# Kernel optimization log

Measured on AMD Instinct MI355X. Metric: run time of the kernel, lower is better.

The kernel has to match this reference:

```python
import jax, jax.numpy as jnp
import numpy as np

N = 65536      # flattened tokens
K = 8192       # codebook_size
D = 64         # codebook_dim
DECAY = 0.9
EPS = 1e-05


def setup_inputs() -> dict:
    key = jax.random.key(0)
    k1, k2, k3, k4 = jax.random.split(key, 4)
    z = jax.random.normal(k1, (N, D), dtype=jnp.float32)
    # codebook initialized uniform(-1, 1) in the torch module
    weight = jax.random.uniform(k2, (K, D), dtype=jnp.float32, minval=-1.0, maxval=1.0)
    # EMA state: positive cluster sizes, embed_avg near the codebook
    cluster_size = jax.random.uniform(k3, (K,), dtype=jnp.float32)
    embed_avg = weight + 0.01 * jax.random.normal(k4, (K, D), dtype=jnp.float32)
    return {"z": z, "weight": weight, "cluster_size": cluster_size, "embed_avg": embed_avg}


def reference(z, weight, cluster_size, embed_avg):
    # VectorQuantizer.ema_update: distances -> argmin -> gather -> EMA stats -> weight refresh
    zd = jax.lax.stop_gradient(z)  # torch uses z.detach() for distance/quant_error
    # distance[n,k] = ||z_n||^2 + ||c_k||^2 - 2 z_n . c_k   (addmm pattern)
    dist = (zd * zd).sum(1, keepdims=True) + (weight * weight).sum(1) - 2.0 * (zd @ weight.T)  # [N, K]
    token = jnp.argmin(dist, axis=1)                      # [N]
    embed = weight[token]                                  # gather [N, D]
    quant_error = jnp.mean(((embed - zd) ** 2).sum(1))

    # onehot_probs.sum(0) == per-code counts; onehot.T @ z == segment sum of z
    counts = jax.ops.segment_sum(jnp.ones((zd.shape[0],), zd.dtype), token, num_segments=K)  # [K]
    embed_sum = jax.ops.segment_sum(z, token, num_segments=K)                                # [K, D]

    new_cluster_size = cluster_size * DECAY + (1.0 - DECAY) * counts
    new_embed_avg = embed_avg * DECAY + (1.0 - DECAY) * embed_sum

    # ema_weight_update with num_tokens = codebook_size
    n = new_cluster_size.sum()
    smoothed = (new_cluster_size + EPS) / (n + K * EPS) * n
    new_weight = new_embed_avg / smoothed[:, None]

    return quant_error, new_weight, new_cluster_size, new_embed_avg
```

## Files before the change

kernel.cpp:

```cpp
#include <hip/hip_runtime.h>
#include <type_traits>

#define N_TOK 65536
#define K_CODE 8192
#define D_DIM 64

constexpr float DECAY = 0.9f;
constexpr float OMD = 0.1f;
constexpr float EPS = 1e-5f;

constexpr int OUT_QE = 0;
constexpr int OUT_W  = 1;
constexpr int OUT_CS = 1 + K_CODE * D_DIM;
constexpr int OUT_EA = OUT_CS + K_CODE;

constexpr int WS_QE     = 0;
constexpr int WS_NSUM   = 16;
constexpr int WS_COUNTS = 16 + 8 * 32;
constexpr int WS_EMBSUM = WS_COUNTS + K_CODE;
constexpr int WS_WHI    = WS_EMBSUM + K_CODE * D_DIM;
constexpr int WS_WLO    = WS_WHI + K_CODE * D_DIM / 2;
constexpr int WS_CNF    = WS_WLO + K_CODE * D_DIM / 2;

typedef __attribute__((ext_vector_type(16))) float floatx16;
typedef __attribute__((ext_vector_type(8)))  short short8;
typedef __attribute__((ext_vector_type(8)))  __bf16 bf16x8;

template <typename T, typename = void> struct mfma_takes : std::false_type {};
template <typename T>
struct mfma_takes<T, std::void_t<decltype(__builtin_amdgcn_mfma_f32_32x32x16_bf16(
    std::declval<T>(), std::declval<T>(), std::declval<floatx16>(), 0, 0, 0))>>
    : std::true_type {};

__device__ __forceinline__ floatx16 MFMA(short8 a, short8 b, floatx16 c) {
  if constexpr (mfma_takes<bf16x8>::value) {
    return __builtin_amdgcn_mfma_f32_32x32x16_bf16(
        __builtin_bit_cast(bf16x8, a), __builtin_bit_cast(bf16x8, b), c, 0, 0, 0);
  } else {
    return __builtin_amdgcn_mfma_f32_32x32x16_bf16(a, b, c, 0, 0, 0);
  }
}

__device__ __forceinline__ unsigned short bf16rne(float x) {
  unsigned int u = __float_as_uint(x);
  return (unsigned short)((u + 0x7FFFu + ((u >> 16) & 1u)) >> 16);
}

__device__ __forceinline__ void gload_lds16(const unsigned short* g, unsigned short* l) {
#if defined(__has_builtin) && __has_builtin(__builtin_amdgcn_global_load_lds)
  typedef __attribute__((address_space(1))) void gvoid;
  typedef __attribute__((address_space(3))) void lvoid;
  __builtin_amdgcn_global_load_lds((gvoid*)g, (lvoid*)l, 16, 0, 0);
#else
  *(uint4*)l = *(const uint4*)g;
#endif
}

__global__ void vq_prep(const float* __restrict__ w, const float* __restrict__ cs,
                        float* __restrict__ ws) {
  const int tid = threadIdx.x;
  const int gid = blockIdx.x * 256 + tid;
  ws[WS_EMBSUM + gid] = 0.0f;
  if (gid < K_CODE) ws[WS_COUNTS + gid] = 0.0f;

  const int d = tid & 63;
  const int kw = tid >> 6;
  const int k = blockIdx.x * 4 + kw;
  const float v = w[(size_t)k * D_DIM + d];
  const unsigned short h = bf16rne(v);
  const float hf = __uint_as_float((unsigned int)h << 16);
  const unsigned short l = bf16rne(v - hf);
  unsigned short* whi = (unsigned short*)(ws + WS_WHI);
  unsigned short* wlo = (unsigned short*)(ws + WS_WLO);
  const int pos = k * D_DIM + (((d >> 3) ^ (k & 7)) * 8) + (d & 7);
  whi[pos] = h;
  wlo[pos] = l;
  float s = v * v;
#pragma unroll
  for (int m = 32; m >= 1; m >>= 1) s += __shfl_xor(s, m);
  __shared__ float csp[4];
  if (d == 0) {
    (ws + WS_CNF)[k] = s + 64.0f;
    csp[kw] = cs[k];
  }
  __syncthreads();
  if (tid == 0) {
    atomicAdd(ws + WS_NSUM + ((blockIdx.x & 7) << 5),
              DECAY * (csp[0] + csp[1] + csp[2] + csp[3]));
  }
}

__global__ __launch_bounds__(512, 4) void vq_argmin(
    const float* __restrict__ z, float* __restrict__ ws)
{
  __shared__ __align__(16) unsigned short Wbuf[2][4][2][32 * 64];
  __shared__ float mind_s[2][128];
  __shared__ int   tok_s[2][128];

  const int tid  = threadIdx.x;
  const int w    = tid >> 6;
  const int lane = tid & 63;
  const int m    = lane & 31;
  const int h    = lane >> 5;
  const int tg   = w & 3;
  const int hw   = w >> 2;
  const int tb   = blockIdx.x * 128;

  const unsigned short* whi = (const unsigned short*)(ws + WS_WHI);
  const unsigned short* wlo = (const unsigned short*)(ws + WS_WLO);
  const float*          cnf = ws + WS_CNF;

  short8 ah[4], al[4];
  float znorm = 0.f;
  {
    const float* zrow = z + (size_t)(tb + tg * 32 + m) * D_DIM + 8 * h;
#pragma unroll
    for (int s4 = 0; s4 < 4; ++s4) {
      const float4 v0 = *(const float4*)(zrow + 16 * s4);
      const float4 v1 = *(const float4*)(zrow + 16 * s4 + 4);
      const float vals[8] = {v0.x, v0.y, v0.z, v0.w, v1.x, v1.y, v1.z, v1.w};
#pragma unroll
      for (int j = 0; j < 8; ++j) {
        const float x = vals[j];
        znorm += x * x;
        const float y = -2.0f * x;
        const unsigned short hb = bf16rne(y);
        const float hf = __uint_as_float((unsigned int)hb << 16);
        const unsigned short lb = bf16rne(y - hf);
        ah[s4][j] = (short)hb;
        al[s4][j] = (short)lb;
      }
    }
    znorm += __shfl_xor(znorm, 32);
  }

  float kmin[16];
#pragma unroll
  for (int r = 0; r < 16; ++r) kmin[r] = 3.4e38f;

  auto issueStage = [&](int sIdx, int bufIdx) {
#pragma unroll
    for (int i = 0; i < 2; ++i) {
      const int t = w * 2 + i;
      const int half = t >> 3, plane = (t >> 2) & 1, seg = t & 3;
      const unsigned short* src = (plane ? wlo : whi)
          + ((size_t)half * 4096 + (size_t)sIdx * 32) * D_DIM + seg * 512 + lane * 8;
      unsigned short* dst = &Wbuf[half][bufIdx][plane][seg * 512];
      gload_lds16(src, dst);
    }
  };

  int xoff[4];
#pragma unroll
  for (int s4 = 0; s4 < 4; ++s4) xoff[s4] = ((2 * s4 + h) ^ (m & 7)) * 8;
  const int mrow = m * 64;
  const int cbase = hw * 4096;

#define RDH(BUF, I) (*(const short8*)&Wbuf[hw][(BUF)][0][mrow + xoff[(I)]])
#define RDL(BUF, I) (*(const short8*)&Wbuf[hw][(BUF)][1][mrow + xoff[(I)]])

  issueStage(0, 0);
  issueStage(1, 1);
  float cn_cur = cnf[cbase + m];
  asm volatile("s_waitcnt vmcnt(0)" ::: "memory");
  __builtin_amdgcn_s_barrier();
  asm volatile("" ::: "memory");

  short8 bh0 = RDH(0, 0), bh1 = RDH(0, 1), bh2 = RDH(0, 2), bh3 = RDH(0, 3);
  short8 bl0 = RDL(0, 0), bl1 = RDL(0, 1), bl2 = RDL(0, 2), bl3 = RDL(0, 3);

  for (int s = 0; s < 128; ++s) {
    issueStage((s + 2) & 127, (s + 2) & 3);
    const float cn_next = cnf[cbase + ((s + 1) & 127) * 32 + m];
    asm volatile("s_waitcnt vmcnt(3)" ::: "memory");
    __builtin_amdgcn_s_barrier();
    asm volatile("" ::: "memory");

    const int nb = (s + 1) & 3;

    floatx16 acc;
#pragma unroll
    for (int r = 0; r < 16; ++r) acc[r] = cn_cur;

    acc = MFMA(ah[0], bh0, acc);
    acc = MFMA(al[0], bh0, acc);
    bh0 = RDH(nb, 0);
    acc = MFMA(ah[1], bh1, acc);
    acc = MFMA(al[1], bh1, acc);
    bh1 = RDH(nb, 1);
    acc = MFMA(ah[2], bh2, acc);
    acc = MFMA(al[2], bh2, acc);
    bh2 = RDH(nb, 2);
    acc = MFMA(ah[3], bh3, acc);
    acc = MFMA(al[3], bh3, acc);
    bh3 = RDH(nb, 3);
    acc = MFMA(ah[0], bl0, acc);
    bl0 = RDL(nb, 0);
    acc = MFMA(ah[1], bl1, acc);
    bl1 = RDL(nb, 1);
    acc = MFMA(ah[2], bl2, acc);
    bl2 = RDL(nb, 2);
    acc = MFMA(ah[3], bl3, acc);
    bl3 = RDL(nb, 3);

#pragma unroll
    for (int r = 0; r < 16; ++r) {
      kmin[r] = fminf(kmin[r],
          __uint_as_float((__float_as_uint(acc[r]) & 0xFFFFFF00u) | (unsigned)s));
    }
    cn_cur = cn_next;
  }
#undef RDH
#undef RDL

#pragma unroll
  for (int r = 0; r < 16; ++r) {
    float kv = kmin[r];
    int mo = m;
#pragma unroll
    for (int mm = 1; mm < 32; mm <<= 1) {
      const float ov = __shfl_xor(kv, mm);
      const int   om = __shfl_xor(mo, mm);
      if (ov < kv || (ov == kv && om < mo)) { kv = ov; mo = om; }
    }
    const int mr = (r & 3) + 8 * (r >> 2) + 4 * h;
    if (m == mr) {
      const unsigned int kb = __float_as_uint(kv);
      tok_s[hw][tg * 32 + mr] = hw * 4096 + (int)(kb & 0xFFu) * 32 + mo;
      mind_s[hw][tg * 32 + mr] =
          __uint_as_float(kb & 0xFFFFFF00u) - 64.0f + znorm;
    }
  }
  __syncthreads();

  float* counts = ws + WS_COUNTS;
  float* embsum = ws + WS_EMBSUM;

  if (tid < 128) {
    const float d0 = mind_s[0][tid], d1 = mind_s[1][tid];
    const int   i0 = tok_s[0][tid],  i1 = tok_s[1][tid];
    const bool t1 = d1 < d0;
    const float dm = t1 ? d1 : d0;
    const int   im = t1 ? i1 : i0;
    tok_s[0][tid] = im;
    float qe = dm;
#pragma unroll
    for (int mm = 32; mm >= 1; mm >>= 1) qe += __shfl_xor(qe, mm);
    if ((tid & 63) == 0) atomicAdd(ws + WS_QE, qe);
    atomicAdd(&counts[im], 1.0f);
  }
  __syncthreads();

#pragma unroll 4
  for (int t = 0; t < 16; ++t) {
    const int row = w * 16 + t;
    const int tk = tok_s[0][row];
    const float zv = z[(size_t)(tb + row) * D_DIM + lane];
    atomicAdd(&embsum[(size_t)tk * D_DIM + lane], zv);
  }
}

__global__ void vq_finalize(const float* __restrict__ cluster_size,
                            const float* __restrict__ embed_avg,
                            const float* __restrict__ ws, float* __restrict__ out)
{
  const int idx = blockIdx.x * 256 + threadIdx.x;
  const int k = idx >> 6;
  const float ncs = cluster_size[k] * DECAY + OMD * ws[WS_COUNTS + k];
  const float nea = embed_avg[idx] * DECAY + OMD * ws[WS_EMBSUM + idx];
  out[OUT_EA + idx] = nea;
  float n = OMD * (float)N_TOK;
#pragma unroll
  for (int i = 0; i < 8; ++i) n += ws[WS_NSUM + (i << 5)];
  const float sm = (ncs + EPS) / (n + K_CODE * EPS) * n;
  out[OUT_W + idx] = nea / sm;
  if ((idx & 63) == 0) out[OUT_CS + k] = ncs;
  if (idx == 0) out[OUT_QE] = ws[WS_QE] * (1.0f / N_TOK);
}

extern "C" void kernel_launch(void* const* d_in, const int* in_sizes, int n_in,
                              void* d_out, int out_size, void* d_ws, size_t ws_size,
                              hipStream_t stream) {
  const float* z  = (const float*)d_in[0];
  const float* w  = (const float*)d_in[1];
  const float* cs = (const float*)d_in[2];
  const float* ea = (const float*)d_in[3];
  float* out = (float*)d_out;
  float* ws  = (float*)d_ws;

  (void)hipMemsetAsync(d_ws, 0, (size_t)WS_COUNTS * sizeof(float), stream);

  vq_prep<<<K_CODE / 4, 256, 0, stream>>>(w, cs, ws);
  vq_argmin<<<N_TOK / 128, 512, 0, stream>>>(z, ws);
  vq_finalize<<<K_CODE * D_DIM / 256, 256, 0, stream>>>(cs, ea, ws, out);
}
```

Baseline: 273.6 us.

## Fuse prep, argmin and finalize into one persistent kernel with grid barriers

```diff
diff --git a/kernel.cpp b/kernel.cpp
--- a/kernel.cpp
+++ b/kernel.cpp
@@ -15,6 +15,8 @@
 constexpr int OUT_EA = OUT_CS + K_CODE;
 
 constexpr int WS_QE     = 0;
+constexpr int WS_BAR0   = 8;
+constexpr int WS_BAR1   = 9;
 constexpr int WS_NSUM   = 16;
 constexpr int WS_COUNTS = 16 + 8 * 32;
 constexpr int WS_EMBSUM = WS_COUNTS + K_CODE;
@@ -56,226 +58,253 @@
 #endif
 }
 
-__global__ void vq_prep(const float* __restrict__ w, const float* __restrict__ cs,
-                        float* __restrict__ ws) {
-  const int tid = threadIdx.x;
-  const int gid = blockIdx.x * 256 + tid;
-  ws[WS_EMBSUM + gid] = 0.0f;
-  if (gid < K_CODE) ws[WS_COUNTS + gid] = 0.0f;
-
-  const int d = tid & 63;
-  const int kw = tid >> 6;
-  const int k = blockIdx.x * 4 + kw;
-  const float v = w[(size_t)k * D_DIM + d];
-  const unsigned short h = bf16rne(v);
-  const float hf = __uint_as_float((unsigned int)h << 16);
-  const unsigned short l = bf16rne(v - hf);
-  unsigned short* whi = (unsigned short*)(ws + WS_WHI);
-  unsigned short* wlo = (unsigned short*)(ws + WS_WLO);
-  const int pos = k * D_DIM + (((d >> 3) ^ (k & 7)) * 8) + (d & 7);
-  whi[pos] = h;
-  wlo[pos] = l;
-  float s = v * v;
-#pragma unroll
-  for (int m = 32; m >= 1; m >>= 1) s += __shfl_xor(s, m);
-  __shared__ float csp[4];
-  if (d == 0) {
-    (ws + WS_CNF)[k] = s + 64.0f;
-    csp[kw] = cs[k];
-  }
+__device__ __forceinline__ void grid_barrier(float* ws, int slot, unsigned nblk) {
   __syncthreads();
-  if (tid == 0) {
-    atomicAdd(ws + WS_NSUM + ((blockIdx.x & 7) << 5),
-              DECAY * (csp[0] + csp[1] + csp[2] + csp[3]));
-  }
-}
-
-__global__ __launch_bounds__(512, 4) void vq_argmin(
-    const float* __restrict__ z, float* __restrict__ ws)
+  if (threadIdx.x == 0) {
+    unsigned int* ctr = (unsigned int*)ws + slot;
+    __threadfence();
+    atomicAdd(ctr, 1u);
+    while (__hip_atomic_load(ctr, __ATOMIC_ACQUIRE, __HIP_MEMORY_SCOPE_AGENT) < nblk) {
+      __builtin_amdgcn_s_sleep(8);
+    }
+    __threadfence();
+  }
+  __syncthreads();
+}
+
+__global__ __launch_bounds__(512, 4) void vq_fused(
+    const float* __restrict__ z, const float* __restrict__ wgt,
+    const float* __restrict__ cs, const float* __restrict__ ea,
+    float* __restrict__ ws, float* __restrict__ out)
 {
   __shared__ __align__(16) unsigned short Wbuf[2][4][2][32 * 64];
   __shared__ float mind_s[2][128];
   __shared__ int   tok_s[2][128];
+  __shared__ float csp[16];
 
   const int tid  = threadIdx.x;
   const int w    = tid >> 6;
   const int lane = tid & 63;
-  const int m    = lane & 31;
-  const int h    = lane >> 5;
-  const int tg   = w & 3;
-  const int hw   = w >> 2;
-  const int tb   = blockIdx.x * 128;
-
-  const unsigned short* whi = (const unsigned short*)(ws + WS_WHI);
-  const unsigned short* wlo = (const unsigned short*)(ws + WS_WLO);
-  const float*          cnf = ws + WS_CNF;
-
-  short8 ah[4], al[4];
-  float znorm = 0.f;
+  const int bid  = blockIdx.x;
+
   {
-    const float* zrow = z + (size_t)(tb + tg * 32 + m) * D_DIM + 8 * h;
-#pragma unroll
-    for (int s4 = 0; s4 < 4; ++s4) {
-      const float4 v0 = *(const float4*)(zrow + 16 * s4);
-      const float4 v1 = *(const float4*)(zrow + 16 * s4 + 4);
-      const float vals[8] = {v0.x, v0.y, v0.z, v0.w, v1.x, v1.y, v1.z, v1.w};
-#pragma unroll
-      for (int j = 0; j < 8; ++j) {
-        const float x = vals[j];
-        znorm += x * x;
-        const float y = -2.0f * x;
-        const unsigned short hb = bf16rne(y);
-        const float hf = __uint_as_float((unsigned int)hb << 16);
-        const unsigned short lb = bf16rne(y - hf);
-        ah[s4][j] = (short)hb;
-        al[s4][j] = (short)lb;
-      }
-    }
-    znorm += __shfl_xor(znorm, 32);
-  }
-
-  float kmin[16];
-#pragma unroll
-  for (int r = 0; r < 16; ++r) kmin[r] = 3.4e38f;
-
-  auto issueStage = [&](int sIdx, int bufIdx) {
-#pragma unroll
-    for (int i = 0; i < 2; ++i) {
-      const int t = w * 2 + i;
-      const int half = t >> 3, plane = (t >> 2) & 1, seg = t & 3;
-      const unsigned short* src = (plane ? wlo : whi)
-          + ((size_t)half * 4096 + (size_t)sIdx * 32) * D_DIM + seg * 512 + lane * 8;
-      unsigned short* dst = &Wbuf[half][bufIdx][plane][seg * 512];
-      gload_lds16(src, dst);
-    }
-  };
-
-  int xoff[4];
-#pragma unroll
-  for (int s4 = 0; s4 < 4; ++s4) xoff[s4] = ((2 * s4 + h) ^ (m & 7)) * 8;
-  const int mrow = m * 64;
-  const int cbase = hw * 4096;
+    ws[WS_EMBSUM + bid * 1024 + tid] = 0.0f;
+    ws[WS_EMBSUM + bid * 1024 + 512 + tid] = 0.0f;
+    if (bid < 16) ws[WS_COUNTS + bid * 512 + tid] = 0.0f;
+
+    unsigned short* whi_w = (unsigned short*)(ws + WS_WHI);
+    unsigned short* wlo_w = (unsigned short*)(ws + WS_WLO);
+#pragma unroll
+    for (int sub = 0; sub < 2; ++sub) {
+      const int k = bid * 16 + w * 2 + sub;
+      const int d = lane;
+      const float v = wgt[(size_t)k * D_DIM + d];
+      const unsigned short hb = bf16rne(v);
+      const float hf = __uint_as_float((unsigned int)hb << 16);
+      const unsigned short lb = bf16rne(v - hf);
+      const int pos = k * D_DIM + (((d >> 3) ^ (k & 7)) * 8) + (d & 7);
+      whi_w[pos] = hb;
+      wlo_w[pos] = lb;
+      float s = v * v;
+#pragma unroll
+      for (int mm = 32; mm >= 1; mm >>= 1) s += __shfl_xor(s, mm);
+      if (d == 0) {
+        (ws + WS_CNF)[k] = s + 64.0f;
+        csp[w * 2 + sub] = cs[k];
+      }
+    }
+    __syncthreads();
+    if (tid == 0) {
+      float t = 0.f;
+#pragma unroll
+      for (int i = 0; i < 16; ++i) t += csp[i];
+      atomicAdd(ws + WS_NSUM + ((bid & 7) << 5), DECAY * t);
+    }
+  }
+
+  grid_barrier(ws, WS_BAR0, 512u);
+
+  {
+    const int m    = lane & 31;
+    const int h    = lane >> 5;
+    const int tg   = w & 3;
+    const int hw   = w >> 2;
+    const int tb   = bid * 128;
+
+    const unsigned short* whi = (const unsigned short*)(ws + WS_WHI);
+    const unsigned short* wlo = (const unsigned short*)(ws + WS_WLO);
+    const float*          cnf = ws + WS_CNF;
+
+    short8 ah[4], al[4];
+    float znorm = 0.f;
+    {
+      const float* zrow = z + (size_t)(tb + tg * 32 + m) * D_DIM + 8 * h;
+#pragma unroll
+      for (int s4 = 0; s4 < 4; ++s4) {
+        const float4 v0 = *(const float4*)(zrow + 16 * s4);
+        const float4 v1 = *(const float4*)(zrow + 16 * s4 + 4);
+        const float vals[8] = {v0.x, v0.y, v0.z, v0.w, v1.x, v1.y, v1.z, v1.w};
+#pragma unroll
+        for (int j = 0; j < 8; ++j) {
+          const float x = vals[j];
+          znorm += x * x;
+          const float y = -2.0f * x;
+          const unsigned short hb = bf16rne(y);
+          const float hf = __uint_as_float((unsigned int)hb << 16);
+          const unsigned short lb = bf16rne(y - hf);
+          ah[s4][j] = (short)hb;
+          al[s4][j] = (short)lb;
+        }
+      }
+      znorm += __shfl_xor(znorm, 32);
+    }
+
+    float kmin[16];
+#pragma unroll
+    for (int r = 0; r < 16; ++r) kmin[r] = 3.4e38f;
+
+    auto issueStage = [&](int sIdx, int bufIdx) {
+#pragma unroll
+      for (int i = 0; i < 2; ++i) {
+        const int t = w * 2 + i;
+        const int half = t >> 3, plane = (t >> 2) & 1, seg = t & 3;
+        const unsigned short* src = (plane ? wlo : whi)
+            + ((size_t)half * 4096 + (size_t)sIdx * 32) * D_DIM + seg * 512 + lane * 8;
+        unsigned short* dst = &Wbuf[half][bufIdx][plane][seg * 512];
+        gload_lds16(src, dst);
+      }
+    };
+
+    int xoff[4];
+#pragma unroll
+    for (int s4 = 0; s4 < 4; ++s4) xoff[s4] = ((2 * s4 + h) ^ (m & 7)) * 8;
+    const int mrow = m * 64;
+    const int cbase = hw * 4096;
 
 #define RDH(BUF, I) (*(const short8*)&Wbuf[hw][(BUF)][0][mrow + xoff[(I)]])
 #define RDL(BUF, I) (*(const short8*)&Wbuf[hw][(BUF)][1][mrow + xoff[(I)]])
 
-  issueStage(0, 0);
-  issueStage(1, 1);
-  float cn_cur = cnf[cbase + m];
-  asm volatile("s_waitcnt vmcnt(0)" ::: "memory");
-  __builtin_amdgcn_s_barrier();
-  asm volatile("" ::: "memory");
-
-  short8 bh0 = RDH(0, 0), bh1 = RDH(0, 1), bh2 = RDH(0, 2), bh3 = RDH(0, 3);
-  short8 bl0 = RDL(0, 0), bl1 = RDL(0, 1), bl2 = RDL(0, 2), bl3 = RDL(0, 3);
-
-  for (int s = 0; s < 128; ++s) {
-    issueStage((s + 2) & 127, (s + 2) & 3);
-    const float cn_next = cnf[cbase + ((s + 1) & 127) * 32 + m];
-    asm volatile("s_waitcnt vmcnt(3)" ::: "memory");
+    issueStage(0, 0);
+    issueStage(1, 1);
+    float cn_cur = cnf[cbase + m];
+    asm volatile("s_waitcnt vmcnt(0)" ::: "memory");
     __builtin_amdgcn_s_barrier();
     asm volatile("" ::: "memory");
 
-    const int nb = (s + 1) & 3;
-
-    floatx16 acc;
-#pragma unroll
-    for (int r = 0; r < 16; ++r) acc[r] = cn_cur;
-
-    acc = MFMA(ah[0], bh0, acc);
-    acc = MFMA(al[0], bh0, acc);
-    bh0 = RDH(nb, 0);
-    acc = MFMA(ah[1], bh1, acc);
-    acc = MFMA(al[1], bh1, acc);
-    bh1 = RDH(nb, 1);
-    acc = MFMA(ah[2], bh2, acc);
-    acc = MFMA(al[2], bh2, acc);
-    bh2 = RDH(nb, 2);
-    acc = MFMA(ah[3], bh3, acc);
-    acc = MFMA(al[3], bh3, acc);
-    bh3 = RDH(nb, 3);
-    acc = MFMA(ah[0], bl0, acc);
-    bl0 = RDL(nb, 0);
-    acc = MFMA(ah[1], bl1, acc);
-    bl1 = RDL(nb, 1);
-    acc = MFMA(ah[2], bl2, acc);
-    bl2 = RDL(nb, 2);
-    acc = MFMA(ah[3], bl3, acc);
-    bl3 = RDL(nb, 3);
-
-#pragma unroll
-    for (int r = 0; r < 16; ++r) {
-      kmin[r] = fminf(kmin[r],
-          __uint_as_float((__float_as_uint(acc[r]) & 0xFFFFFF00u) | (unsigned)s));
-    }
-    cn_cur = cn_next;
-  }
+    short8 bh0 = RDH(0, 0), bh1 = RDH(0, 1), bh2 = RDH(0, 2), bh3 = RDH(0, 3);
+    short8 bl0 = RDL(0, 0), bl1 = RDL(0, 1), bl2 = RDL(0, 2), bl3 = RDL(0, 3);
+
+    for (int s = 0; s < 128; ++s) {
+      issueStage((s + 2) & 127, (s + 2) & 3);
+      const float cn_next = cnf[cbase + ((s + 1) & 127) * 32 + m];
+      asm volatile("s_waitcnt vmcnt(3)" ::: "memory");
+      __builtin_amdgcn_s_barrier();
+      asm volatile("" ::: "memory");
+
+      const int nb = (s + 1) & 3;
+
+      floatx16 acc;
+#pragma unroll
+      for (int r = 0; r < 16; ++r) acc[r] = cn_cur;
+
+      acc = MFMA(ah[0], bh0, acc);
+      acc = MFMA(al[0], bh0, acc);
+      bh0 = RDH(nb, 0);
+      acc = MFMA(ah[1], bh1, acc);
+      acc = MFMA(al[1], bh1, acc);
+      bh1 = RDH(nb, 1);
+      acc = MFMA(ah[2], bh2, acc);
+      acc = MFMA(al[2], bh2, acc);
+      bh2 = RDH(nb, 2);
+      acc = MFMA(ah[3], bh3, acc);
+      acc = MFMA(al[3], bh3, acc);
+      bh3 = RDH(nb, 3);
+      acc = MFMA(ah[0], bl0, acc);
+      bl0 = RDL(nb, 0);
+      acc = MFMA(ah[1], bl1, acc);
+      bl1 = RDL(nb, 1);
+      acc = MFMA(ah[2], bl2, acc);
+      bl2 = RDL(nb, 2);
+      acc = MFMA(ah[3], bl3, acc);
+      bl3 = RDL(nb, 3);
+
+#pragma unroll
+      for (int r = 0; r < 16; ++r) {
+        kmin[r] = fminf(kmin[r],
+            __uint_as_float((__float_as_uint(acc[r]) & 0xFFFFFF00u) | (unsigned)s));
+      }
+      cn_cur = cn_next;
+    }
 #undef RDH
 #undef RDL
 
 #pragma unroll
-  for (int r = 0; r < 16; ++r) {
-    float kv = kmin[r];
-    int mo = m;
-#pragma unroll
-    for (int mm = 1; mm < 32; mm <<= 1) {
-      const float ov = __shfl_xor(kv, mm);
-      const int   om = __shfl_xor(mo, mm);
-      if (ov < kv || (ov == kv && om < mo)) { kv = ov; mo = om; }
-    }
-    const int mr = (r & 3) + 8 * (r >> 2) + 4 * h;
-    if (m == mr) {
-      const unsigned int kb = __float_as_uint(kv);
-      tok_s[hw][tg * 32 + mr] = hw * 4096 + (int)(kb & 0xFFu) * 32 + mo;
-      mind_s[hw][tg * 32 + mr] =
-          __uint_as_float(kb & 0xFFFFFF00u) - 64.0f + znorm;
-    }
-  }
-  __syncthreads();
-
-  float* counts = ws + WS_COUNTS;
-  float* embsum = ws + WS_EMBSUM;
-
-  if (tid < 128) {
-    const float d0 = mind_s[0][tid], d1 = mind_s[1][tid];
-    const int   i0 = tok_s[0][tid],  i1 = tok_s[1][tid];
-    const bool t1 = d1 < d0;
-    const float dm = t1 ? d1 : d0;
-    const int   im = t1 ? i1 : i0;
-    tok_s[0][tid] = im;
-    float qe = dm;
-#pragma unroll
-    for (int mm = 32; mm >= 1; mm >>= 1) qe += __shfl_xor(qe, mm);
-    if ((tid & 63) == 0) atomicAdd(ws + WS_QE, qe);
-    atomicAdd(&counts[im], 1.0f);
-  }
-  __syncthreads();
+    for (int r = 0; r < 16; ++r) {
+      float kv = kmin[r];
+      int mo = m;
+#pragma unroll
+      for (int mm = 1; mm < 32; mm <<= 1) {
+        const float ov = __shfl_xor(kv, mm);
+        const int   om = __shfl_xor(mo, mm);
+        if (ov < kv || (ov == kv && om < mo)) { kv = ov; mo = om; }
+      }
+      const int mr = (r & 3) + 8 * (r >> 2) + 4 * h;
+      if (m == mr) {
+        const unsigned int kb = __float_as_uint(kv);
+        tok_s[hw][tg * 32 + mr] = hw * 4096 + (int)(kb & 0xFFu) * 32 + mo;
+        mind_s[hw][tg * 32 + mr] =
+            __uint_as_float(kb & 0xFFFFFF00u) - 64.0f + znorm;
+      }
+    }
+    __syncthreads();
+
+    float* counts = ws + WS_COUNTS;
+    float* embsum = ws + WS_EMBSUM;
+
+    if (tid < 128) {
+      const float d0 = mind_s[0][tid], d1 = mind_s[1][tid];
+      const int   i0 = tok_s[0][tid],  i1 = tok_s[1][tid];
+      const bool t1 = d1 < d0;
+      const float dm = t1 ? d1 : d0;
+      const int   im = t1 ? i1 : i0;
+      tok_s[0][tid] = im;
+      float qe = dm;
+#pragma unroll
+      for (int mm = 32; mm >= 1; mm >>= 1) qe += __shfl_xor(qe, mm);
+      if ((tid & 63) == 0) atomicAdd(ws + WS_QE, qe);
+      atomicAdd(&counts[im], 1.0f);
+    }
+    __syncthreads();
 
 #pragma unroll 4
-  for (int t = 0; t < 16; ++t) {
-    const int row = w * 16 + t;
-    const int tk = tok_s[0][row];
-    const float zv = z[(size_t)(tb + row) * D_DIM + lane];
-    atomicAdd(&embsum[(size_t)tk * D_DIM + lane], zv);
-  }
-}
-
-__global__ void vq_finalize(const float* __restrict__ cluster_size,
-                            const float* __restrict__ embed_avg,
-                            const float* __restrict__ ws, float* __restrict__ out)
-{
-  const int idx = blockIdx.x * 256 + threadIdx.x;
-  const int k = idx >> 6;
-  const float ncs = cluster_size[k] * DECAY + OMD * ws[WS_COUNTS + k];
-  const float nea = embed_avg[idx] * DECAY + OMD * ws[WS_EMBSUM + idx];
-  out[OUT_EA + idx] = nea;
-  float n = OMD * (float)N_TOK;
-#pragma unroll
-  for (int i = 0; i < 8; ++i) n += ws[WS_NSUM + (i << 5)];
-  const float sm = (ncs + EPS) / (n + K_CODE * EPS) * n;
-  out[OUT_W + idx] = nea / sm;
-  if ((idx & 63) == 0) out[OUT_CS + k] = ncs;
-  if (idx == 0) out[OUT_QE] = ws[WS_QE] * (1.0f / N_TOK);
+    for (int t = 0; t < 16; ++t) {
+      const int row = w * 16 + t;
+      const int tk = tok_s[0][row];
+      const float zv = z[(size_t)(tb + row) * D_DIM + lane];
+      atomicAdd(&embsum[(size_t)tk * D_DIM + lane], zv);
+    }
+  }
+
+  grid_barrier(ws, WS_BAR1, 512u);
+
+  {
+    float n = OMD * (float)N_TOK;
+#pragma unroll
+    for (int i = 0; i < 8; ++i) n += ws[WS_NSUM + (i << 5)];
+    const float inv_den = n / (n + K_CODE * EPS);
+#pragma unroll
+    for (int j = 0; j < 2; ++j) {
+      const int idx = bid * 1024 + j * 512 + tid;
+      const int k = idx >> 6;
+      const float ncs = cs[k] * DECAY + OMD * ws[WS_COUNTS + k];
+      const float nea = ea[idx] * DECAY + OMD * ws[WS_EMBSUM + idx];
+      out[OUT_EA + idx] = nea;
+      const float sm = (ncs + EPS) * inv_den;
+      out[OUT_W + idx] = nea / sm;
+      if ((idx & 63) == 0) out[OUT_CS + k] = ncs;
+    }
+    if (bid == 0 && tid == 0) out[OUT_QE] = ws[WS_QE] * (1.0f / N_TOK);
+  }
 }
 
 extern "C" void kernel_launch(void* const* d_in, const int* in_sizes, int n_in,
@@ -290,7 +319,5 @@
 
   (void)hipMemsetAsync(d_ws, 0, (size_t)WS_COUNTS * sizeof(float), stream);
 
-  vq_prep<<<K_CODE / 4, 256, 0, stream>>>(w, cs, ws);
-  vq_argmin<<<N_TOK / 128, 512, 0, stream>>>(z, ws);
-  vq_finalize<<<K_CODE * D_DIM / 256, 256, 0, stream>>>(cs, ea, ws, out);
-}
+  vq_fused<<<512, 512, 0, stream>>>(z, w, cs, ea, ws, out);
+}
```

After: 479.5 us. 75.2% more time.
